# Kernel optimization log

Hardware: AMD Instinct MI355X
Metric: run time of the kernel (lower is better)

The kernel has to match this reference:

```python
import jax, jax.numpy as jnp
import numpy as np

N_NODES = 50000
N_EDGES = 800000
IN_DIM = 512
HEADS = 4
OUT_DIM = 64


def setup_inputs() -> dict:
    key = jax.random.key(0)
    k1, k2, k3, k4 = jax.random.split(key, 4)
    x = jax.random.normal(k1, (N_NODES, IN_DIM), dtype=jnp.float32)
    edges = jax.random.randint(k2, (N_EDGES, 2), 0, N_NODES, dtype=jnp.int32)
    W = jax.random.normal(k3, (IN_DIM, HEADS * OUT_DIM), dtype=jnp.float32) * 0.05
    a = jax.random.normal(k4, (HEADS, 2 * OUT_DIM), dtype=jnp.float32) * 0.05
    bias = jnp.zeros((HEADS * OUT_DIM,), dtype=jnp.float32)
    return {"x": x, "edges": edges, "W": W, "a": a, "bias": bias}


def reference(x, edges, W, a, bias):
    num_nodes = x.shape[0]
    # project: [N, H, D]
    h = (x @ W).reshape(num_nodes, HEADS, OUT_DIM)
    src = edges[:, 0]
    dst = edges[:, 1]
    # raw attention per edge, per head: e = sum(a * concat(h_src, h_dst))
    a_src = a[:, :OUT_DIM]   # [H, D]
    a_dst = a[:, OUT_DIM:]   # [H, D]
    # precompute per-node dot-products, then gather (avoids [E,H,2D] concat)
    s_src = jnp.einsum('nhd,hd->nh', h, a_src)  # [N, H]
    s_dst = jnp.einsum('nhd,hd->nh', h, a_dst)  # [N, H]
    e = s_src[src] + s_dst[dst]                 # [E, H]
    e = jax.nn.leaky_relu(e, negative_slope=0.2)
    # softmax over edges grouped by SOURCE node (as in original code)
    max_e = jax.ops.segment_max(e, src, num_segments=num_nodes)  # [N, H]
    exp_e = jnp.exp(e - max_e[src])
    sum_exp = jax.ops.segment_sum(exp_e, src, num_segments=num_nodes)
    alpha = exp_e / (sum_exp[src] + 1e-10)       # [E, H]
    # messages aggregated at DESTINATION node
    messages = alpha[:, :, None] * h[src]        # [E, H, D]
    out = jax.ops.segment_sum(messages, dst, num_segments=num_nodes)  # [N, H, D]
    out = out.reshape(num_nodes, HEADS * OUT_DIM) + bias
    return out
```

## Files before the change

### kernel.cpp

```cpp
#include <hip/hip_runtime.h>
#include <math.h>

#define IN_DIM 512
#define NH 4
#define OD 64
#define HD 256

typedef float  floatx4 __attribute__((ext_vector_type(4)));
typedef short  shortx8 __attribute__((ext_vector_type(8)));

__device__ __forceinline__ unsigned short f2bf(float x) {
    unsigned int u = __float_as_uint(x);
    u += 0x7fffu + ((u >> 16) & 1u);
    return (unsigned short)(u >> 16);
}
__device__ __forceinline__ float bf2f(unsigned short u) {
    return __uint_as_float(((unsigned int)u) << 16);
}

__global__ void prep_kernel(const float* __restrict__ W, ushort* __restrict__ Wt,
                            int* __restrict__ head_src, int* __restrict__ head_dst,
                            int M) {
    int t = blockIdx.x * blockDim.x + threadIdx.x;
    if (t < 16 * M) head_src[t] = -1;
    if (t < 8 * M) head_dst[t] = -1;
    if (t < 256 * 64) {
        int n = t >> 6;
        int k8 = (t & 63) * 8;
        shortx8 v;
        #pragma unroll
        for (int j = 0; j < 8; ++j) v[j] = (short)f2bf(W[(size_t)(k8 + j) * HD + n]);
        *(shortx8*)&Wt[(size_t)n * IN_DIM + k8] = v;
    }
}

__global__ __launch_bounds__(256) void gemm_kernel(const float* __restrict__ x,
                                                   const ushort* __restrict__ Wt,
                                                   ushort* __restrict__ h,
                                                   const float* __restrict__ a,
                                                   float2* __restrict__ ssi,
                                                   float* __restrict__ s_dst,
                                                   int M) {
    __shared__ ushort As[64 * 64];
    __shared__ ushort Bs[256 * 64];
    const int tid = threadIdx.x;
    const int lane = tid & 63;
    const int w = tid >> 6;
    const int bm = blockIdx.x * 64;
    const int wn = w * 64;
    const int lm = lane & 15;
    const int lq = lane >> 4;
    floatx4 acc[4][4];
    #pragma unroll
    for (int i = 0; i < 4; ++i)
        #pragma unroll
        for (int j = 0; j < 4; ++j) acc[i][j] = (floatx4){0.f, 0.f, 0.f, 0.f};

    for (int k0 = 0; k0 < IN_DIM; k0 += 64) {
        #pragma unroll
        for (int j = 0; j < 2; ++j) {
            int ch = tid * 2 + j;
            int row = ch >> 3;
            int c = (ch & 7) ^ (row & 7);
            int gr = bm + row;
            shortx8 v = (shortx8){0, 0, 0, 0, 0, 0, 0, 0};
            if (gr < M) {
                const float* gp = &x[(size_t)gr * IN_DIM + k0 + c * 8];
                float4 v0 = *(const float4*)gp;
                float4 v1 = *(const float4*)(gp + 4);
                v[0] = (short)f2bf(v0.x); v[1] = (short)f2bf(v0.y);
                v[2] = (short)f2bf(v0.z); v[3] = (short)f2bf(v0.w);
                v[4] = (short)f2bf(v1.x); v[5] = (short)f2bf(v1.y);
                v[6] = (short)f2bf(v1.z); v[7] = (short)f2bf(v1.w);
            }
            *(shortx8*)&As[ch * 8] = v;
        }
        #pragma unroll
        for (int j = 0; j < 8; ++j) {
            int ch = j * 256 + tid;
            int row = ch >> 3;
            int c = (ch & 7) ^ (row & 7);
            const ushort* gp = &Wt[(size_t)row * IN_DIM + k0 + c * 8];
            __builtin_amdgcn_global_load_lds(
                (const __attribute__((address_space(1))) void*)gp,
                (__attribute__((address_space(3))) void*)&Bs[(size_t)(j * 256 + wn) * 8],
                16, 0, 0);
        }
        __syncthreads();
        #pragma unroll
        for (int kk = 0; kk < 2; ++kk) {
            shortx8 af[4], bfr[4];
            #pragma unroll
            for (int mt = 0; mt < 4; ++mt) {
                int row = mt * 16 + lm;
                int c = (kk * 4 + lq) ^ (row & 7);
                af[mt] = *(const shortx8*)&As[row * 64 + c * 8];
            }
            #pragma unroll
            for (int nt = 0; nt < 4; ++nt) {
                int row = wn + nt * 16 + lm;
                int c = (kk * 4 + lq) ^ (row & 7);
                bfr[nt] = *(const shortx8*)&Bs[row * 64 + c * 8];
            }
            #pragma unroll
            for (int mt = 0; mt < 4; ++mt)
                #pragma unroll
                for (int nt = 0; nt < 4; ++nt)
                    acc[mt][nt] = __builtin_amdgcn_mfma_f32_16x16x32_bf16(
                        af[mt], bfr[nt], acc[mt][nt], 0, 0, 0);
        }
        __syncthreads();
    }
    float as_l[4], ad_l[4];
    #pragma unroll
    for (int nt = 0; nt < 4; ++nt) {
        as_l[nt] = a[w * 2 * OD + nt * 16 + lm];
        ad_l[nt] = a[w * 2 * OD + OD + nt * 16 + lm];
    }
    #pragma unroll
    for (int mt = 0; mt < 4; ++mt)
        #pragma unroll
        for (int r = 0; r < 4; ++r) {
            float ps = 0.f, pd = 0.f;
            #pragma unroll
            for (int nt = 0; nt < 4; ++nt) {
                float v = acc[mt][nt][r];
                ps += v * as_l[nt];
                pd += v * ad_l[nt];
            }
            #pragma unroll
            for (int off = 1; off < 16; off <<= 1) {
                ps += __shfl_xor(ps, off, 64);
                pd += __shfl_xor(pd, off, 64);
            }
            int m = bm + mt * 16 + lq * 4 + r;
            if (m < M && lm == 0) {
                ssi[m * NH + w].x = ps;
                s_dst[m * NH + w] = pd;
            }
        }
    #pragma unroll
    for (int mt = 0; mt < 4; ++mt)
        #pragma unroll
        for (int r = 0; r < 4; ++r) {
            int m = bm + mt * 16 + lq * 4 + r;
            if (m < M) {
                #pragma unroll
                for (int nt = 0; nt < 4; ++nt)
                    h[(size_t)m * HD + wn + nt * 16 + lm] = f2bf(acc[mt][nt][r]);
            }
        }
}

__global__ void link_kernel(const int2* __restrict__ edges,
                            int* __restrict__ head_src, int2* __restrict__ next_src,
                            int* __restrict__ head_dst, int2* __restrict__ next_dst,
                            int E) {
    int i = blockIdx.x * blockDim.x + threadIdx.x;
    if (i >= E) return;
    int2 e = edges[i];
    int ps = atomicExch(&head_src[16 * e.x + (i & 15)], i);
    next_src[i] = make_int2(ps, e.y);
    int pd = atomicExch(&head_dst[8 * e.y + (i & 7)], i);
    next_dst[i] = make_int2(pd, e.x);
}

__global__ __launch_bounds__(256) void src_sum_kernel(const int* __restrict__ head_src,
                                                      const int2* __restrict__ next_src,
                                                      float2* __restrict__ ssi,
                                                      const float* __restrict__ s_dst, int M) {
    int lane = threadIdx.x & 63;
    int n = blockIdx.x * 4 + (threadIdx.x >> 6);
    if (n >= M) return;
    int slot = lane >> 2;
    int hd = lane & 3;
    float ss = ssi[n * NH + hd].x;
    float sum = 0.f;
    int e = head_src[16 * n + slot];
    while (e != -1) {
        int2 t = next_src[e];
        float sd = s_dst[t.y * NH + hd];
        float a0 = ss + sd;
        a0 = a0 > 0.f ? a0 : 0.2f * a0;
        sum += __expf(a0);
        e = t.x;
    }
    sum += __shfl_xor(sum, 4, 64);
    sum += __shfl_xor(sum, 8, 64);
    sum += __shfl_xor(sum, 16, 64);
    sum += __shfl_xor(sum, 32, 64);
    if (lane < 4) ssi[n * NH + lane].y = 1.f / (sum + 1e-10f);
}

__global__ __launch_bounds__(256) void gather_kernel(const int* __restrict__ head_dst,
                              const int2* __restrict__ next_dst,
                              const float2* __restrict__ ssi,
                              const float* __restrict__ s_dst,
                              const ushort* __restrict__ h,
                              const float* __restrict__ bias,
                              float* __restrict__ out, int M) {
    int lane = threadIdx.x & 63;
    int n = blockIdx.x * 4 + (threadIdx.x >> 6);
    if (n >= M) return;
    int half = lane >> 5;
    int l5 = lane & 31;
    int head = l5 >> 3;
    int c0 = l5 * 8;
    float sdst = s_dst[n * NH + head];
    floatx4 accA = {0.f, 0.f, 0.f, 0.f}, accB = {0.f, 0.f, 0.f, 0.f};
    int e0 = head_dst[8 * n + 4 * half + 0];
    int e1 = head_dst[8 * n + 4 * half + 1];
    int e2 = head_dst[8 * n + 4 * half + 2];
    int e3 = head_dst[8 * n + 4 * half + 3];

    while (e0 != -1 || e1 != -1 || e2 != -1 || e3 != -1) {
        bool b0 = e0 != -1, b1 = e1 != -1, b2 = e2 != -1, b3 = e3 != -1;
        int2 t0, t1, t2, t3;
        if (b0) t0 = next_dst[e0];
        if (b1) t1 = next_dst[e1];
        if (b2) t2 = next_dst[e2];
        if (b3) t3 = next_dst[e3];
        float2 si0, si1, si2, si3;
        shortx8 h0, h1, h2, h3;
        if (b0) { si0 = ssi[(size_t)t0.y * NH + head]; h0 = *(const shortx8*)&h[(size_t)t0.y * HD + c0]; }
        if (b1) { si1 = ssi[(size_t)t1.y * NH + head]; h1 = *(const shortx8*)&h[(size_t)t1.y * HD + c0]; }
        if (b2) { si2 = ssi[(size_t)t2.y * NH + head]; h2 = *(const shortx8*)&h[(size_t)t2.y * HD + c0]; }
        if (b3) { si3 = ssi[(size_t)t3.y * NH + head]; h3 = *(const shortx8*)&h[(size_t)t3.y * HD + c0]; }
#define GAT_EDGE(B, SI, HU, EV, TV) do {                                       \
        if (B) {                                                               \
            float es_ = (SI).x + sdst;                                         \
            es_ = es_ > 0.f ? es_ : 0.2f * es_;                                \
            float al_ = __expf(es_) * (SI).y;                                  \
            accA.x += al_ * bf2f((ushort)(HU)[0]);                             \
            accA.y += al_ * bf2f((ushort)(HU)[1]);                             \
            accA.z += al_ * bf2f((ushort)(HU)[2]);                             \
            accA.w += al_ * bf2f((ushort)(HU)[3]);                             \
            accB.x += al_ * bf2f((ushort)(HU)[4]);                             \
            accB.y += al_ * bf2f((ushort)(HU)[5]);                             \
            accB.z += al_ * bf2f((ushort)(HU)[6]);                             \
            accB.w += al_ * bf2f((ushort)(HU)[7]);                             \
            EV = (TV).x;                                                       \
        }                                                                      \
    } while (0)
        GAT_EDGE(b0, si0, h0, e0, t0);
        GAT_EDGE(b1, si1, h1, e1, t1);
        GAT_EDGE(b2, si2, h2, e2, t2);
        GAT_EDGE(b3, si3, h3, e3, t3);
#undef GAT_EDGE
    }

    accA.x += __shfl_xor(accA.x, 32, 64); accA.y += __shfl_xor(accA.y, 32, 64);
    accA.z += __shfl_xor(accA.z, 32, 64); accA.w += __shfl_xor(accA.w, 32, 64);
    accB.x += __shfl_xor(accB.x, 32, 64); accB.y += __shfl_xor(accB.y, 32, 64);
    accB.z += __shfl_xor(accB.z, 32, 64); accB.w += __shfl_xor(accB.w, 32, 64);
    if (half == 0) {
        float4 b0 = *(const float4*)&bias[c0];
        float4 b1 = *(const float4*)&bias[c0 + 4];
        float4 o0 = make_float4(accA.x + b0.x, accA.y + b0.y, accA.z + b0.z, accA.w + b0.w);
        float4 o1 = make_float4(accB.x + b1.x, accB.y + b1.y, accB.z + b1.z, accB.w + b1.w);
        *(float4*)&out[(size_t)n * HD + c0] = o0;
        *(float4*)&out[(size_t)n * HD + c0 + 4] = o1;
    }
}

extern "C" void kernel_launch(void* const* d_in, const int* in_sizes, int n_in,
                              void* d_out, int out_size, void* d_ws, size_t ws_size,
                              hipStream_t stream) {
    const float* x     = (const float*)d_in[0];
    const int2*  edges = (const int2*)d_in[1];
    const float* W     = (const float*)d_in[2];
    const float* a     = (const float*)d_in[3];
    const float* bias  = (const float*)d_in[4];
    float* out = (float*)d_out;
    const int M = in_sizes[0] / IN_DIM;
    const int E = in_sizes[1] / 2;

    char* p = (char*)d_ws;
    ushort* hB       = (ushort*)p; p += (size_t)M * HD * sizeof(ushort);
    ushort* Wt       = (ushort*)p; p += (size_t)HD * IN_DIM * sizeof(ushort);
    float*  s_dst    = (float*)p;  p += (size_t)M * NH * sizeof(float);
    float2* ssi      = (float2*)p; p += (size_t)M * NH * sizeof(float2);
    int*    head_src = (int*)p;    p += (size_t)16 * M * sizeof(int);
    int*    head_dst = (int*)p;    p += (size_t)8 * M * sizeof(int);
    int2*   next_src = (int2*)p;   p += (size_t)E * sizeof(int2);
    int2*   next_dst = (int2*)p;   p += (size_t)E * sizeof(int2);

    prep_kernel<<<(16 * M + 255) / 256, 256, 0, stream>>>(W, Wt, head_src, head_dst, M);
    gemm_kernel<<<(M + 63) / 64, 256, 0, stream>>>(x, Wt, hB, a, ssi, s_dst, M);
    link_kernel<<<(E + 255) / 256, 256, 0, stream>>>(edges, head_src, next_src,
                                                     head_dst, next_dst, E);
    src_sum_kernel<<<(M + 3) / 4, 256, 0, stream>>>(head_src, next_src, ssi, s_dst, M);
    gather_kernel<<<(M + 3) / 4, 256, 0, stream>>>(head_dst, next_dst, ssi, s_dst,
                                                   hB, bias, out, M);
}
```

Measured before the change: 361.9 us.

## Pre-convert x to bf16 in a fused prep/link kernel and DMA it into LDS

```diff
diff --git a/kernel.cpp b/kernel.cpp
--- a/kernel.cpp
+++ b/kernel.cpp
@@ -18,12 +18,27 @@
     return __uint_as_float(((unsigned int)u) << 16);
 }
 
-__global__ void prep_kernel(const float* __restrict__ W, ushort* __restrict__ Wt,
-                            int* __restrict__ head_src, int* __restrict__ head_dst,
+__global__ void init_kernel(int* __restrict__ head_src, int* __restrict__ head_dst,
                             int M) {
     int t = blockIdx.x * blockDim.x + threadIdx.x;
     if (t < 16 * M) head_src[t] = -1;
     if (t < 8 * M) head_dst[t] = -1;
+}
+
+__global__ void prep_link_kernel(const float* __restrict__ W, ushort* __restrict__ Wt,
+                                 const float* __restrict__ x, ushort* __restrict__ xb,
+                                 const int2* __restrict__ edges,
+                                 int* __restrict__ head_src, int2* __restrict__ next_src,
+                                 int* __restrict__ head_dst, int2* __restrict__ next_dst,
+                                 int M, int E) {
+    int t = blockIdx.x * blockDim.x + threadIdx.x;
+    if (t < E) {
+        int2 e = edges[t];
+        int ps = atomicExch(&head_src[16 * e.x + (t & 15)], t);
+        next_src[t] = make_int2(ps, e.y);
+        int pd = atomicExch(&head_dst[8 * e.y + (t & 7)], t);
+        next_dst[t] = make_int2(pd, e.x);
+    }
     if (t < 256 * 64) {
         int n = t >> 6;
         int k8 = (t & 63) * 8;
@@ -32,9 +47,24 @@
         for (int j = 0; j < 8; ++j) v[j] = (short)f2bf(W[(size_t)(k8 + j) * HD + n]);
         *(shortx8*)&Wt[(size_t)n * IN_DIM + k8] = v;
     }
-}
-
+    if (xb && t < M * 64) {
+        int row = t >> 6;
+        int k8 = (t & 63) * 8;
+        const float* gp = &x[(size_t)row * IN_DIM + k8];
+        float4 v0 = *(const float4*)gp;
+        float4 v1 = *(const float4*)(gp + 4);
+        shortx8 v;
+        v[0] = (short)f2bf(v0.x); v[1] = (short)f2bf(v0.y);
+        v[2] = (short)f2bf(v0.z); v[3] = (short)f2bf(v0.w);
+        v[4] = (short)f2bf(v1.x); v[5] = (short)f2bf(v1.y);
+        v[6] = (short)f2bf(v1.z); v[7] = (short)f2bf(v1.w);
+        *(shortx8*)&xb[(size_t)row * IN_DIM + k8] = v;
+    }
+}
+
+template<bool XB>
 __global__ __launch_bounds__(256) void gemm_kernel(const float* __restrict__ x,
+                                                   const ushort* __restrict__ xb,
                                                    const ushort* __restrict__ Wt,
                                                    ushort* __restrict__ h,
                                                    const float* __restrict__ a,
@@ -57,23 +87,37 @@
         for (int j = 0; j < 4; ++j) acc[i][j] = (floatx4){0.f, 0.f, 0.f, 0.f};
 
     for (int k0 = 0; k0 < IN_DIM; k0 += 64) {
-        #pragma unroll
-        for (int j = 0; j < 2; ++j) {
-            int ch = tid * 2 + j;
-            int row = ch >> 3;
-            int c = (ch & 7) ^ (row & 7);
-            int gr = bm + row;
-            shortx8 v = (shortx8){0, 0, 0, 0, 0, 0, 0, 0};
-            if (gr < M) {
-                const float* gp = &x[(size_t)gr * IN_DIM + k0 + c * 8];
-                float4 v0 = *(const float4*)gp;
-                float4 v1 = *(const float4*)(gp + 4);
-                v[0] = (short)f2bf(v0.x); v[1] = (short)f2bf(v0.y);
-                v[2] = (short)f2bf(v0.z); v[3] = (short)f2bf(v0.w);
-                v[4] = (short)f2bf(v1.x); v[5] = (short)f2bf(v1.y);
-                v[6] = (short)f2bf(v1.z); v[7] = (short)f2bf(v1.w);
-            }
-            *(shortx8*)&As[ch * 8] = v;
+        if constexpr (XB) {
+            #pragma unroll
+            for (int j = 0; j < 2; ++j) {
+                int ch = j * 256 + tid;
+                int row = ch >> 3;
+                int c = (ch & 7) ^ (row & 7);
+                const ushort* gp = &xb[(size_t)(bm + row) * IN_DIM + k0 + c * 8];
+                __builtin_amdgcn_global_load_lds(
+                    (const __attribute__((address_space(1))) void*)gp,
+                    (__attribute__((address_space(3))) void*)&As[(size_t)(j * 256 + wn) * 8],
+                    16, 0, 0);
+            }
+        } else {
+            #pragma unroll
+            for (int j = 0; j < 2; ++j) {
+                int ch = tid * 2 + j;
+                int row = ch >> 3;
+                int c = (ch & 7) ^ (row & 7);
+                int gr = bm + row;
+                shortx8 v = (shortx8){0, 0, 0, 0, 0, 0, 0, 0};
+                if (gr < M) {
+                    const float* gp = &x[(size_t)gr * IN_DIM + k0 + c * 8];
+                    float4 v0 = *(const float4*)gp;
+                    float4 v1 = *(const float4*)(gp + 4);
+                    v[0] = (short)f2bf(v0.x); v[1] = (short)f2bf(v0.y);
+                    v[2] = (short)f2bf(v0.z); v[3] = (short)f2bf(v0.w);
+                    v[4] = (short)f2bf(v1.x); v[5] = (short)f2bf(v1.y);
+                    v[6] = (short)f2bf(v1.z); v[7] = (short)f2bf(v1.w);
+                }
+                *(shortx8*)&As[ch * 8] = v;
+            }
         }
         #pragma unroll
         for (int j = 0; j < 8; ++j) {
@@ -150,19 +194,6 @@
                     h[(size_t)m * HD + wn + nt * 16 + lm] = f2bf(acc[mt][nt][r]);
             }
         }
-}
-
-__global__ void link_kernel(const int2* __restrict__ edges,
-                            int* __restrict__ head_src, int2* __restrict__ next_src,
-                            int* __restrict__ head_dst, int2* __restrict__ next_dst,
-                            int E) {
-    int i = blockIdx.x * blockDim.x + threadIdx.x;
-    if (i >= E) return;
-    int2 e = edges[i];
-    int ps = atomicExch(&head_src[16 * e.x + (i & 15)], i);
-    next_src[i] = make_int2(ps, e.y);
-    int pd = atomicExch(&head_dst[8 * e.y + (i & 7)], i);
-    next_dst[i] = make_int2(pd, e.x);
 }
 
 __global__ __launch_bounds__(256) void src_sum_kernel(const int* __restrict__ head_src,
@@ -276,19 +307,30 @@
     const int E = in_sizes[1] / 2;
 
     char* p = (char*)d_ws;
-    ushort* hB       = (ushort*)p; p += (size_t)M * HD * sizeof(ushort);
-    ushort* Wt       = (ushort*)p; p += (size_t)HD * IN_DIM * sizeof(ushort);
-    float*  s_dst    = (float*)p;  p += (size_t)M * NH * sizeof(float);
-    float2* ssi      = (float2*)p; p += (size_t)M * NH * sizeof(float2);
-    int*    head_src = (int*)p;    p += (size_t)16 * M * sizeof(int);
-    int*    head_dst = (int*)p;    p += (size_t)8 * M * sizeof(int);
-    int2*   next_src = (int2*)p;   p += (size_t)E * sizeof(int2);
-    int2*   next_dst = (int2*)p;   p += (size_t)E * sizeof(int2);
-
-    prep_kernel<<<(16 * M + 255) / 256, 256, 0, stream>>>(W, Wt, head_src, head_dst, M);
-    gemm_kernel<<<(M + 63) / 64, 256, 0, stream>>>(x, Wt, hB, a, ssi, s_dst, M);
-    link_kernel<<<(E + 255) / 256, 256, 0, stream>>>(edges, head_src, next_src,
-                                                     head_dst, next_dst, E);
+    auto alloc = [&](size_t bytes) { char* q = p; p += (bytes + 255) & ~(size_t)255; return q; };
+    ushort* hB       = (ushort*)alloc((size_t)M * HD * sizeof(ushort));
+    ushort* Wt       = (ushort*)alloc((size_t)HD * IN_DIM * sizeof(ushort));
+    float*  s_dst    = (float*)alloc((size_t)M * NH * sizeof(float));
+    float2* ssi      = (float2*)alloc((size_t)M * NH * sizeof(float2));
+    int*    head_src = (int*)alloc((size_t)16 * M * sizeof(int));
+    int*    head_dst = (int*)alloc((size_t)8 * M * sizeof(int));
+    int2*   next_src = (int2*)alloc((size_t)E * sizeof(int2));
+    int2*   next_dst = (int2*)alloc((size_t)E * sizeof(int2));
+    size_t xb_bytes = (size_t)(M + 64) * IN_DIM * sizeof(ushort);
+    ushort* xb = nullptr;
+    if ((size_t)(p - (char*)d_ws) + xb_bytes <= ws_size)
+        xb = (ushort*)alloc(xb_bytes);
+
+    init_kernel<<<(16 * M + 255) / 256, 256, 0, stream>>>(head_src, head_dst, M);
+    int pl_threads = xb ? (M * 64) : (E > 256 * 64 ? E : 256 * 64);
+    prep_link_kernel<<<(pl_threads + 255) / 256, 256, 0, stream>>>(
+        W, Wt, x, xb, edges, head_src, next_src, head_dst, next_dst, M, E);
+    if (xb)
+        gemm_kernel<true><<<(M + 63) / 64, 256, 0, stream>>>(x, xb, Wt, hB, a,
+                                                             ssi, s_dst, M);
+    else
+        gemm_kernel<false><<<(M + 63) / 64, 256, 0, stream>>>(x, xb, Wt, hB, a,
+                                                              ssi, s_dst, M);
     src_sum_kernel<<<(M + 3) / 4, 256, 0, stream>>>(head_src, next_src, ssi, s_dst, M);
     gather_kernel<<<(M + 3) / 4, 256, 0, stream>>>(head_dst, next_dst, ssi, s_dst,
                                                    hB, bias, out, M);
```

Result: slower. 371.0 us (+2.5%).
